# Performance work log

Hardware: AMD Instinct MI355X
Metric: run time of the kernel (lower is better)

The kernel has to match this reference:

```python
import jax, jax.numpy as jnp
import numpy as np

SLIDING_WINDOW = 2048
NUM_SINK = 4


def make_mask(q_len, k_len, dtype=jnp.float32):
    # positions of queries in the key axis
    q_pos = jnp.arange(k_len - q_len, k_len)[:, None]  # [Q,1]
    k_pos = jnp.arange(k_len)[None, :]                 # [1,K]
    causal = k_pos <= q_pos
    in_window = k_pos >= (q_pos - SLIDING_WINDOW + 1)
    is_sink = k_pos < NUM_SINK
    allowed = causal & (in_window | is_sink)
    return jnp.where(allowed, jnp.zeros((), dtype), jnp.full((), -jnp.inf, dtype))


def setup_inputs() -> dict:
    key = jax.random.key(0)
    k1, k2, k3 = jax.random.split(key, 3)
    B, H, L, D = 2, 16, 4096, 128
    q = jax.random.normal(k1, (B, H, L, D), dtype=jnp.float32)
    k = jax.random.normal(k2, (B, H, L, D), dtype=jnp.float32)
    v = jax.random.normal(k3, (B, H, L, D), dtype=jnp.float32)
    return {"q": q, "k": k, "v": v}


def reference(q, k, v):
    B, H, L, D = q.shape
    mask = make_mask(L, k.shape[2], q.dtype)  # [L, L] additive
    scale = 1.0 / jnp.sqrt(jnp.asarray(D, q.dtype))
    scores = jnp.einsum('bhqd,bhkd->bhqk', q, k) * scale + mask
    probs = jax.nn.softmax(scores, axis=-1)
    return jnp.einsum('bhqk,bhkd->bhqd', probs, v)
```

## Files before the change

kernel.cpp:

```cpp
#include <hip/hip_runtime.h>

constexpr int Ld = 4096;
constexpr int Dd = 128;
constexpr int BQ = 128;
constexpr int BK = 64;
constexpr int WSZ = 2048;
constexpr int NSINK = 4;
constexpr float QSCALE = 0.08838834764831845f * 1.4426950408889634f;

typedef short bf16x8 __attribute__((ext_vector_type(8)));
typedef float f32x4 __attribute__((ext_vector_type(4)));

#if defined(__has_builtin)
#if __has_builtin(__builtin_amdgcn_exp2f)
#define EXP2(x) __builtin_amdgcn_exp2f(x)
#endif
#endif
#ifndef EXP2
#define EXP2(x) exp2f(x)
#endif

__device__ __forceinline__ unsigned pkbf(float hi, float lo) {
    unsigned r;
    asm("v_cvt_pk_bf16_f32 %0, %1, %2" : "=v"(r) : "v"(lo), "v"(hi));
    return r;
}

__device__ __forceinline__ int rd_off(int row, int d) {
    return row * 128 + ((((d >> 3) ^ row) & 15) << 3) + (d & 7);
}
__device__ __forceinline__ int vt_off(int drow, int key) {
    return drow * 64 + ((((key >> 3) ^ drow) & 7) << 3) + (key & 7);
}
__device__ __forceinline__ int p_off(int row, int key) {
    return row * 64 + ((((key >> 2) ^ ((row & 7) << 1)) & 15) << 2) + (key & 3);
}

__global__ __launch_bounds__(256, 2)
void swa_fwd(const float* __restrict__ Qg, const float* __restrict__ Kg,
             const float* __restrict__ Vg, float* __restrict__ Og) {
    __shared__ __align__(16) unsigned short smem[24576];
    unsigned short* Ks  = smem;
    unsigned short* Vts = smem + 8192;
    unsigned short* Ps  = smem + 16384;
    unsigned short* Qst = smem;

    const int tid  = threadIdx.x;
    const int w    = tid >> 6;
    const int lane = tid & 63;
    const int ml   = lane & 15;
    const int quad = lane >> 4;

    const int qtile = (int)(gridDim.x - 1u - blockIdx.x);
    const int q0 = qtile * BQ;
    const int bh = blockIdx.y;

    const size_t baseQ  = ((size_t)bh * Ld + q0) * Dd;
    const size_t baseKV = (size_t)bh * Ld * Dd;

    #pragma unroll
    for (int i = 0; i < 16; ++i) {
        int idx = tid + i * 256;
        int row = idx >> 5;
        int d0  = (idx & 31) << 2;
        float4 v = *(const float4*)(Qg + baseQ + (size_t)row * Dd + d0);
        *(uint2*)&Qst[rd_off(row, d0)] =
            make_uint2(pkbf(v.y * QSCALE, v.x * QSCALE),
                       pkbf(v.w * QSCALE, v.z * QSCALE));
    }
    __syncthreads();

    bf16x8 qf[2][4];
    #pragma unroll
    for (int g = 0; g < 2; ++g)
        #pragma unroll
        for (int k0 = 0; k0 < 4; ++k0)
            qf[g][k0] = *(const bf16x8*)&Qst[rd_off(w * 32 + g * 16 + ml,
                                                    k0 * 32 + quad * 8)];

    float m_i[2] = {-3e38f, -3e38f};
    float l_i[2] = {0.f, 0.f};
    f32x4 o_acc[2][8];
    #pragma unroll
    for (int g = 0; g < 2; ++g)
        #pragma unroll
        for (int dt = 0; dt < 8; ++dt)
            o_acc[g][dt] = (f32x4){0.f, 0.f, 0.f, 0.f};

    const int kmin = (q0 - (WSZ - 1)) > 0 ? (q0 - (WSZ - 1)) : 0;
    const int kb_first = (kmin / BK) * BK;
    const bool sink_extra = (kb_first > 0);
    const int nch = (q0 + BQ - kb_first) / BK + (sink_extra ? 1 : 0);

    const int qrow0 = q0 + w * 32 + ml;
    unsigned short* Pw = Ps + w * 2048;

    float4 kreg[8];
    float  vreg[32];
    const int kr0 = tid >> 5;
    const int kd0 = (tid & 31) << 2;
    const int vd  = tid & 127;
    const int vkh = tid >> 7;

    auto kvload = [&](int kb) {
        const float* kp = Kg + baseKV + (size_t)(kb + kr0) * Dd + kd0;
        #pragma unroll
        for (int i = 0; i < 8; ++i)
            kreg[i] = *(const float4*)(kp + (size_t)i * 8 * Dd);
        const float* vp = Vg + baseKV + (size_t)(kb + vkh * 32) * Dd + vd;
        #pragma unroll
        for (int j = 0; j < 32; ++j)
            vreg[j] = vp[(size_t)j * Dd];
    };
    auto kb_of = [&](int ci) {
        return sink_extra ? (ci == 0 ? 0 : kb_first + (ci - 1) * BK)
                          : kb_first + ci * BK;
    };

    kvload(kb_of(0));

    for (int ci = 0; ci < nch; ++ci) {
        const int kb = kb_of(ci);

        __syncthreads();

        #pragma unroll
        for (int i = 0; i < 8; ++i)
            *(uint2*)&Ks[rd_off(kr0 + i * 8, kd0)] =
                make_uint2(pkbf(kreg[i].y, kreg[i].x),
                           pkbf(kreg[i].w, kreg[i].z));
        #pragma unroll
        for (int m2 = 0; m2 < 4; ++m2) {
            *(uint4*)&Vts[vt_off(vd, vkh * 32 + m2 * 8)] =
                make_uint4(pkbf(vreg[m2 * 8 + 1], vreg[m2 * 8 + 0]),
                           pkbf(vreg[m2 * 8 + 3], vreg[m2 * 8 + 2]),
                           pkbf(vreg[m2 * 8 + 5], vreg[m2 * 8 + 4]),
                           pkbf(vreg[m2 * 8 + 7], vreg[m2 * 8 + 6]));
        }
        __syncthreads();

        if (ci + 1 < nch) kvload(kb_of(ci + 1));

        f32x4 s[2][4];
        #pragma unroll
        for (int g = 0; g < 2; ++g)
            #pragma unroll
            for (int t = 0; t < 4; ++t)
                s[g][t] = (f32x4){0.f, 0.f, 0.f, 0.f};
        #pragma unroll
        for (int k0 = 0; k0 < 4; ++k0) {
            bf16x8 ka[4];
            #pragma unroll
            for (int t = 0; t < 4; ++t)
                ka[t] = *(const bf16x8*)&Ks[rd_off(t * 16 + ml, k0 * 32 + quad * 8)];
            #pragma unroll
            for (int t = 0; t < 4; ++t) {
                s[0][t] = __builtin_amdgcn_mfma_f32_16x16x32_bf16(ka[t], qf[0][k0], s[0][t], 0, 0, 0);
                s[1][t] = __builtin_amdgcn_mfma_f32_16x16x32_bf16(ka[t], qf[1][k0], s[1][t], 0, 0, 0);
            }
        }

        const bool full = (kb + (BK - 1) <= q0) && (kb + (WSZ - BQ) >= q0 - 1);

        #pragma unroll
        for (int g = 0; g < 2; ++g) {
            const int q = qrow0 + g * 16;
            if (!full) {
                #pragma unroll
                for (int t = 0; t < 4; ++t)
                    #pragma unroll
                    for (int r = 0; r < 4; ++r) {
                        int k = kb + t * 16 + quad * 4 + r;
                        bool ok = (k <= q) && ((k + (WSZ - 1) >= q) || (k < NSINK));
                        s[g][t][r] = ok ? s[g][t][r] : -3e38f;
                    }
            }
            float mx = s[g][0][0];
            #pragma unroll
            for (int t = 0; t < 4; ++t)
                #pragma unroll
                for (int r = 0; r < 4; ++r) mx = fmaxf(mx, s[g][t][r]);
            mx = fmaxf(mx, __shfl_xor(mx, 16));
            mx = fmaxf(mx, __shfl_xor(mx, 32));
            const float mnew = fmaxf(m_i[g], mx);
            const float alpha = EXP2(m_i[g] - mnew);
            m_i[g] = mnew;
            float rs = 0.f;
            #pragma unroll
            for (int t = 0; t < 4; ++t)
                #pragma unroll
                for (int r = 0; r < 4; ++r) {
                    float p = EXP2(s[g][t][r] - mnew);
                    s[g][t][r] = p;
                    rs += p;
                }
            rs += __shfl_xor(rs, 16);
            rs += __shfl_xor(rs, 32);
            l_i[g] = alpha * l_i[g] + rs;

            unsigned short* Pg = Pw + g * 1024;
            #pragma unroll
            for (int t = 0; t < 4; ++t)
                *(uint2*)&Pg[p_off(ml, t * 16 + quad * 4)] =
                    make_uint2(pkbf(s[g][t][1], s[g][t][0]),
                               pkbf(s[g][t][3], s[g][t][2]));
            #pragma unroll
            for (int dt = 0; dt < 8; ++dt) o_acc[g][dt] *= alpha;
        }

        #pragma unroll
        for (int k0 = 0; k0 < 2; ++k0) {
            bf16x8 pb0 = *(const bf16x8*)&Pw[p_off(ml, k0 * 32 + quad * 8)];
            bf16x8 pb1 = *(const bf16x8*)&Pw[1024 + p_off(ml, k0 * 32 + quad * 8)];
            #pragma unroll
            for (int dt = 0; dt < 8; ++dt) {
                bf16x8 va = *(const bf16x8*)&Vts[vt_off(dt * 16 + ml, k0 * 32 + quad * 8)];
                o_acc[0][dt] = __builtin_amdgcn_mfma_f32_16x16x32_bf16(va, pb0, o_acc[0][dt], 0, 0, 0);
                o_acc[1][dt] = __builtin_amdgcn_mfma_f32_16x16x32_bf16(va, pb1, o_acc[1][dt], 0, 0, 0);
            }
        }
    }

    #pragma unroll
    for (int g = 0; g < 2; ++g) {
        const float inv = 1.f / l_i[g];
        float* op = Og + ((size_t)bh * Ld + (qrow0 + g * 16)) * Dd;
        #pragma unroll
        for (int dt = 0; dt < 8; ++dt) {
            float4 o;
            o.x = o_acc[g][dt][0] * inv;
            o.y = o_acc[g][dt][1] * inv;
            o.z = o_acc[g][dt][2] * inv;
            o.w = o_acc[g][dt][3] * inv;
            *(float4*)(op + dt * 16 + quad * 4) = o;
        }
    }
}

extern "C" void kernel_launch(void* const* d_in, const int* in_sizes, int n_in,
                              void* d_out, int out_size, void* d_ws, size_t ws_size,
                              hipStream_t stream) {
    const float* q = (const float*)d_in[0];
    const float* k = (const float*)d_in[1];
    const float* v = (const float*)d_in[2];
    float* o = (float*)d_out;
    const int bhn = in_sizes[0] / (Ld * Dd);
    dim3 grid(Ld / BQ, bhn);
    swa_fwd<<<grid, dim3(256, 1, 1), 0, stream>>>(q, k, v, o);
}
```

Baseline: 411.2 us.

## Pre-convert K/V to swizzled bf16 tiles and DMA them into LDS

Adds a prep kernel that converts K and V once to bf16, already swizzled and with V transposed, into per-chunk workspace images. The attention kernel then pulls K straight into LDS with global_load_lds DMA and copies V tiles as plain 16-byte vectors. This removes the repeated fp32 loads and conversions of overlapping K/V windows done by every query tile, and it loads Q directly into registers. The cost is an extra launch, workspace traffic and a different barrier placement; a fallback path keeps the old kernel when the workspace is too small.

Result: slower. 672.3 us (+63.5%).

```diff
diff --git a/kernel.cpp b/kernel.cpp
--- a/kernel.cpp
+++ b/kernel.cpp
@@ -36,9 +36,248 @@
     return row * 64 + ((((key >> 2) ^ ((row & 7) << 1)) & 15) << 2) + (key & 3);
 }
 
+typedef const __attribute__((address_space(1))) void* gas_p;
+typedef __attribute__((address_space(3))) void* las_p;
+__device__ __forceinline__ void dma16(const void* g, void* l) {
+    __builtin_amdgcn_global_load_lds((gas_p)g, (las_p)l, 16, 0, 0);
+}
+
+__global__ __launch_bounds__(256, 4)
+void prep(const float* __restrict__ Kg, const float* __restrict__ Vg,
+          unsigned short* __restrict__ Wk, unsigned short* __restrict__ Wv) {
+    __shared__ __align__(16) unsigned short Vst[8192];
+    const int c = blockIdx.x, bh = blockIdx.y, tid = threadIdx.x;
+    const size_t src = ((size_t)bh * Ld + c * 64) * Dd;
+    unsigned short* kimg = Wk + (((size_t)bh * 64 + c) << 13);
+    unsigned short* vimg = Wv + (((size_t)bh * 64 + c) << 13);
+
+    #pragma unroll
+    for (int i = 0; i < 4; ++i) {
+        int idx = tid + i * 256;
+        int row = idx >> 4;
+        int d0  = (((idx & 15) ^ row) & 15) << 3;
+        const float* kp = Kg + src + (size_t)row * Dd + d0;
+        float4 a = *(const float4*)kp;
+        float4 b = *(const float4*)(kp + 4);
+        *(uint4*)&kimg[idx * 8] =
+            make_uint4(pkbf(a.y, a.x), pkbf(a.w, a.z),
+                       pkbf(b.y, b.x), pkbf(b.w, b.z));
+    }
+    {
+        int d  = tid & 127;
+        int kh = tid >> 7;
+        const float* vp = Vg + src + (size_t)(kh * 32) * Dd + d;
+        #pragma unroll
+        for (int m2 = 0; m2 < 4; ++m2) {
+            float e0 = vp[(m2 * 8 + 0) * Dd], e1 = vp[(m2 * 8 + 1) * Dd];
+            float e2 = vp[(m2 * 8 + 2) * Dd], e3 = vp[(m2 * 8 + 3) * Dd];
+            float e4 = vp[(m2 * 8 + 4) * Dd], e5 = vp[(m2 * 8 + 5) * Dd];
+            float e6 = vp[(m2 * 8 + 6) * Dd], e7 = vp[(m2 * 8 + 7) * Dd];
+            *(uint4*)&Vst[vt_off(d, kh * 32 + m2 * 8)] =
+                make_uint4(pkbf(e1, e0), pkbf(e3, e2),
+                           pkbf(e5, e4), pkbf(e7, e6));
+        }
+    }
+    __syncthreads();
+    #pragma unroll
+    for (int i = 0; i < 4; ++i) {
+        int idx = tid + i * 256;
+        *(uint4*)&vimg[idx * 8] = *(const uint4*)&Vst[idx * 8];
+    }
+}
+
+__global__ __launch_bounds__(256, 3)
+void swa_fwd(const float* __restrict__ Qg,
+             const unsigned short* __restrict__ Wk,
+             const unsigned short* __restrict__ Wv,
+             float* __restrict__ Og) {
+    __shared__ __align__(16) unsigned short Ks[8192];
+    __shared__ __align__(16) unsigned short Vts[8192];
+    __shared__ __align__(16) unsigned short Ps[8192];
+
+    const int tid  = threadIdx.x;
+    const int w    = tid >> 6;
+    const int lane = tid & 63;
+    const int ml   = lane & 15;
+    const int quad = lane >> 4;
+
+    const int qtile = (int)(gridDim.x - 1u - blockIdx.x);
+    const int q0 = qtile * BQ;
+    const int bh = blockIdx.y;
+
+    bf16x8 qf[2][4];
+    #pragma unroll
+    for (int g = 0; g < 2; ++g) {
+        const float* qp = Qg + ((size_t)bh * Ld + q0 + w * 32 + g * 16 + ml) * Dd;
+        #pragma unroll
+        for (int k0 = 0; k0 < 4; ++k0) {
+            const float* p = qp + k0 * 32 + quad * 8;
+            float4 a = *(const float4*)p;
+            float4 b = *(const float4*)(p + 4);
+            uint4 u = make_uint4(
+                pkbf(a.y * QSCALE, a.x * QSCALE), pkbf(a.w * QSCALE, a.z * QSCALE),
+                pkbf(b.y * QSCALE, b.x * QSCALE), pkbf(b.w * QSCALE, b.z * QSCALE));
+            qf[g][k0] = *(bf16x8*)&u;
+        }
+    }
+
+    float m_i[2] = {-3e38f, -3e38f};
+    float l_i[2] = {0.f, 0.f};
+    f32x4 o_acc[2][8];
+    #pragma unroll
+    for (int g = 0; g < 2; ++g)
+        #pragma unroll
+        for (int dt = 0; dt < 8; ++dt)
+            o_acc[g][dt] = (f32x4){0.f, 0.f, 0.f, 0.f};
+
+    const int kmin = (q0 - (WSZ - 1)) > 0 ? (q0 - (WSZ - 1)) : 0;
+    const int kb_first = (kmin / BK) * BK;
+    const bool sink_extra = (kb_first > 0);
+    const int nch = (q0 + BQ - kb_first) / BK + (sink_extra ? 1 : 0);
+    auto kb_of = [&](int ci) {
+        return sink_extra ? (ci == 0 ? 0 : kb_first + (ci - 1) * BK)
+                          : kb_first + ci * BK;
+    };
+
+    const unsigned short* kim0 = Wk + ((size_t)bh << 19);
+    const unsigned short* vim0 = Wv + ((size_t)bh << 19);
+
+    uint4 vr[4];
+    {
+        const int c0 = kb_of(0) >> 6;
+        const unsigned short* kg = kim0 + ((size_t)c0 << 13) + w * 2048 + lane * 8;
+        #pragma unroll
+        for (int i = 0; i < 4; ++i)
+            dma16(kg + i * 512, &Ks[w * 2048 + i * 512]);
+        const uint4* vg = (const uint4*)(vim0 + ((size_t)c0 << 13));
+        #pragma unroll
+        for (int i = 0; i < 4; ++i) vr[i] = vg[tid + i * 256];
+    }
+
+    const int qrow0 = q0 + w * 32 + ml;
+    unsigned short* Pw = Ps + w * 2048;
+
+    for (int ci = 0; ci < nch; ++ci) {
+        const int kb = kb_of(ci);
+
+        __syncthreads();
+
+        #pragma unroll
+        for (int i = 0; i < 4; ++i)
+            *(uint4*)&Vts[(tid + i * 256) * 8] = vr[i];
+
+        f32x4 s[2][4];
+        #pragma unroll
+        for (int g = 0; g < 2; ++g)
+            #pragma unroll
+            for (int t = 0; t < 4; ++t)
+                s[g][t] = (f32x4){0.f, 0.f, 0.f, 0.f};
+        #pragma unroll
+        for (int k0 = 0; k0 < 4; ++k0) {
+            bf16x8 ka[4];
+            #pragma unroll
+            for (int t = 0; t < 4; ++t)
+                ka[t] = *(const bf16x8*)&Ks[rd_off(t * 16 + ml, k0 * 32 + quad * 8)];
+            #pragma unroll
+            for (int t = 0; t < 4; ++t) {
+                s[0][t] = __builtin_amdgcn_mfma_f32_16x16x32_bf16(ka[t], qf[0][k0], s[0][t], 0, 0, 0);
+                s[1][t] = __builtin_amdgcn_mfma_f32_16x16x32_bf16(ka[t], qf[1][k0], s[1][t], 0, 0, 0);
+            }
+        }
+
+        __syncthreads();
+
+        if (ci + 1 < nch) {
+            const int c2 = kb_of(ci + 1) >> 6;
+            const unsigned short* kg = kim0 + ((size_t)c2 << 13) + w * 2048 + lane * 8;
+            #pragma unroll
+            for (int i = 0; i < 4; ++i)
+                dma16(kg + i * 512, &Ks[w * 2048 + i * 512]);
+            const uint4* vg = (const uint4*)(vim0 + ((size_t)c2 << 13));
+            #pragma unroll
+            for (int i = 0; i < 4; ++i) vr[i] = vg[tid + i * 256];
+        }
+
+        const bool full = (kb + (BK - 1) <= q0) && (kb + (WSZ - BQ) >= q0 - 1);
+
+        #pragma unroll
+        for (int g = 0; g < 2; ++g) {
+            const int q = qrow0 + g * 16;
+            if (!full) {
+                #pragma unroll
+                for (int t = 0; t < 4; ++t)
+                    #pragma unroll
+                    for (int r = 0; r < 4; ++r) {
+                        int k = kb + t * 16 + quad * 4 + r;
+                        bool ok = (k <= q) && ((k + (WSZ - 1) >= q) || (k < NSINK));
+                        s[g][t][r] = ok ? s[g][t][r] : -3e38f;
+                    }
+            }
+            float mx = s[g][0][0];
+            #pragma unroll
+            for (int t = 0; t < 4; ++t)
+                #pragma unroll
+                for (int r = 0; r < 4; ++r) mx = fmaxf(mx, s[g][t][r]);
+            mx = fmaxf(mx, __shfl_xor(mx, 16));
+            mx = fmaxf(mx, __shfl_xor(mx, 32));
+            const float mnew = fmaxf(m_i[g], mx);
+            const float alpha = EXP2(m_i[g] - mnew);
+            m_i[g] = mnew;
+            float rs = 0.f;
+            #pragma unroll
+            for (int t = 0; t < 4; ++t)
+                #pragma unroll
+                for (int r = 0; r < 4; ++r) {
+                    float p = EXP2(s[g][t][r] - mnew);
+                    s[g][t][r] = p;
+                    rs += p;
+                }
+            rs += __shfl_xor(rs, 16);
+            rs += __shfl_xor(rs, 32);
+            l_i[g] = alpha * l_i[g] + rs;
+
+            unsigned short* Pg = Pw + g * 1024;
+            #pragma unroll
+            for (int t = 0; t < 4; ++t)
+                *(uint2*)&Pg[p_off(ml, t * 16 + quad * 4)] =
+                    make_uint2(pkbf(s[g][t][1], s[g][t][0]),
+                               pkbf(s[g][t][3], s[g][t][2]));
+            #pragma unroll
+            for (int dt = 0; dt < 8; ++dt) o_acc[g][dt] *= alpha;
+        }
+
+        #pragma unroll
+        for (int k0 = 0; k0 < 2; ++k0) {
+            bf16x8 pb0 = *(const bf16x8*)&Pw[p_off(ml, k0 * 32 + quad * 8)];
+            bf16x8 pb1 = *(const bf16x8*)&Pw[1024 + p_off(ml, k0 * 32 + quad * 8)];
+            #pragma unroll
+            for (int dt = 0; dt < 8; ++dt) {
+                bf16x8 va = *(const bf16x8*)&Vts[vt_off(dt * 16 + ml, k0 * 32 + quad * 8)];
+                o_acc[0][dt] = __builtin_amdgcn_mfma_f32_16x16x32_bf16(va, pb0, o_acc[0][dt], 0, 0, 0);
+                o_acc[1][dt] = __builtin_amdgcn_mfma_f32_16x16x32_bf16(va, pb1, o_acc[1][dt], 0, 0, 0);
+            }
+        }
+    }
+
+    #pragma unroll
+    for (int g = 0; g < 2; ++g) {
+        const float inv = 1.f / l_i[g];
+        float* op = Og + ((size_t)bh * Ld + (qrow0 + g * 16)) * Dd;
+        #pragma unroll
+        for (int dt = 0; dt < 8; ++dt) {
+            float4 o;
+            o.x = o_acc[g][dt][0] * inv;
+            o.y = o_acc[g][dt][1] * inv;
+            o.z = o_acc[g][dt][2] * inv;
+            o.w = o_acc[g][dt][3] * inv;
+            *(float4*)(op + dt * 16 + quad * 4) = o;
+        }
+    }
+}
+
 __global__ __launch_bounds__(256, 2)
-void swa_fwd(const float* __restrict__ Qg, const float* __restrict__ Kg,
-             const float* __restrict__ Vg, float* __restrict__ Og) {
+void swa_fwd_fb(const float* __restrict__ Qg, const float* __restrict__ Kg,
+                const float* __restrict__ Vg, float* __restrict__ Og) {
     __shared__ __align__(16) unsigned short smem[24576];
     unsigned short* Ks  = smem;
     unsigned short* Vts = smem + 8192;
@@ -121,9 +360,7 @@
 
     for (int ci = 0; ci < nch; ++ci) {
         const int kb = kb_of(ci);
-
         __syncthreads();
-
         #pragma unroll
         for (int i = 0; i < 8; ++i)
             *(uint2*)&Ks[rd_off(kr0 + i * 8, kd0)] =
@@ -138,7 +375,6 @@
                            pkbf(vreg[m2 * 8 + 7], vreg[m2 * 8 + 6]));
         }
         __syncthreads();
-
         if (ci + 1 < nch) kvload(kb_of(ci + 1));
 
         f32x4 s[2][4];
@@ -245,6 +481,13 @@
     const float* v = (const float*)d_in[2];
     float* o = (float*)d_out;
     const int bhn = in_sizes[0] / (Ld * Dd);
-    dim3 grid(Ld / BQ, bhn);
-    swa_fwd<<<grid, dim3(256, 1, 1), 0, stream>>>(q, k, v, o);
-}
+    const size_t need = (size_t)bhn * 64 * 8192 * 2  * 2 ;
+    if (ws_size >= need) {
+        unsigned short* Wk = (unsigned short*)d_ws;
+        unsigned short* Wv = Wk + (size_t)bhn * 64 * 8192;
+        prep<<<dim3(Ld / 64, bhn), dim3(256, 1, 1), 0, stream>>>(k, v, Wk, Wv);
+        swa_fwd<<<dim3(Ld / BQ, bhn), dim3(256, 1, 1), 0, stream>>>(q, Wk, Wv, o);
+    } else {
+        swa_fwd_fb<<<dim3(Ld / BQ, bhn), dim3(256, 1, 1), 0, stream>>>(q, k, v, o);
+    }
+}
```
